# Optimization experiments

Hardware: AMD Instinct MI355X
Metric: run time of the kernel (lower is better)

## Reference

```python
import jax, jax.numpy as jnp
import numpy as np

WS = (7, 7)  # window size
NUM_HEADS = 16


def _relative_position_index(ws):
    # Deterministic int index table, computed exactly as in the torch module.
    coords = np.stack(np.meshgrid(np.arange(ws[0]), np.arange(ws[1]), indexing='ij'))  # [2,Wh,Ww]
    coords = coords.reshape(2, -1)                       # [2, N]
    rel = coords[:, :, None] - coords[:, None, :]        # [2, N, N]
    rel = rel.transpose(1, 2, 0)                         # [N, N, 2]
    rel = rel + np.array([ws[0] - 1, ws[1] - 1])
    rel[:, :, 0] *= 2 * ws[1] - 1
    return jnp.asarray(rel.sum(-1), dtype=jnp.int32)     # [N, N]


def setup_inputs() -> dict:
    key = jax.random.key(0)
    ks = jax.random.split(key, 5)
    B_, N, C = 2048, WS[0] * WS[1], 512
    nw = 64
    return {
        'x': jax.random.normal(ks[0], (B_, N, C), dtype=jnp.float32),
        'mask': jax.random.normal(ks[1], (nw, N, N), dtype=jnp.float32),
        'qkv_w': jax.random.normal(ks[2], (3 * C, C), dtype=jnp.float32) * 0.02,
        'qkv_b': jax.random.normal(ks[3], (3 * C,), dtype=jnp.float32) * 0.02,
        'rpb_table': jax.random.normal(ks[4], ((2 * WS[0] - 1) * (2 * WS[1] - 1), NUM_HEADS), dtype=jnp.float32) * 0.02,
    }


def reference(x, mask, qkv_w, qkv_b, rpb_table):
    B_, N, C = x.shape
    H = NUM_HEADS
    hd = C // H
    scale = hd ** -0.5

    # qkv projection: [B_, N, 3, H, hd] -> q, k, v each [B_, H, N, hd]
    qkv = (jnp.einsum('bnc,oc->bno', x, qkv_w) + qkv_b)
    qkv = qkv.reshape(B_, N, 3, H, hd).transpose(2, 0, 3, 1, 4)
    q, k, v = qkv[0], qkv[1], qkv[2]

    attn = jnp.einsum('bhnd,bhmd->bhnm', q * scale, k)  # [B_, H, N, N]

    rel_idx = _relative_position_index(WS)                       # [N, N]
    bias = rpb_table[rel_idx.reshape(-1)].reshape(N, N, H)       # gather
    attn = attn + bias.transpose(2, 0, 1)[None]                  # [1, H, N, N]

    nw = mask.shape[0]
    attn = attn.reshape(B_ // nw, nw, H, N, N) + mask[None, :, None]
    attn = attn.reshape(B_, H, N, N)
    attn = jax.nn.softmax(attn, axis=-1)

    out = jnp.einsum('bhnm,bhmd->bhnd', attn, v)
    out = out.transpose(0, 2, 1, 3).reshape(B_, N, C)
    # NOTE: source assigns `X = self.proj(x)` but returns `x`, so the
    # output projection is dead code; we faithfully return pre-proj output.
    return out
```

## Files before the change

### kernel.cpp

```cpp
#include <hip/hip_runtime.h>
#include <cstdint>
#include <cstddef>

typedef __bf16 bf16x8 __attribute__((ext_vector_type(8)));
typedef float f32x4 __attribute__((ext_vector_type(4)));
typedef unsigned short u16x8 __attribute__((ext_vector_type(8)));
typedef unsigned short u16x4 __attribute__((ext_vector_type(4)));
typedef unsigned int u32x2 __attribute__((ext_vector_type(2)));

#define VT_LD 56
#define LDE 144
#define BSTRIDE 52
#define BSZ 2548
#define PLD 80

__device__ __forceinline__ unsigned short f2bf(float f) {
  unsigned int u = __builtin_bit_cast(unsigned int, f);
  u += 0x7FFFu + ((u >> 16) & 1u);
  return (unsigned short)(u >> 16);
}
__device__ __forceinline__ float bf2f(unsigned short h) {
  unsigned int u = (unsigned int)h << 16;
  return __builtin_bit_cast(float, u);
}

__device__ __forceinline__ void gload_lds16(const void* g, void* l) {
  __builtin_amdgcn_global_load_lds((const __attribute__((address_space(1))) void*)g,
                                   (__attribute__((address_space(3))) void*)l, 16, 0, 0);
}

__global__ void conv_f2b_k(const float* __restrict__ src, unsigned short* __restrict__ dst, long n8) {
  long i = (long)blockIdx.x * blockDim.x + threadIdx.x;
  long stride = (long)gridDim.x * blockDim.x;
  for (; i < n8; i += stride) {
    float4 a = *(const float4*)(src + i * 8);
    float4 b = *(const float4*)(src + i * 8 + 4);
    u16x8 p;
    p[0]=f2bf(a.x); p[1]=f2bf(a.y); p[2]=f2bf(a.z); p[3]=f2bf(a.w);
    p[4]=f2bf(b.x); p[5]=f2bf(b.y); p[6]=f2bf(b.z); p[7]=f2bf(b.w);
    *(u16x8*)(dst + i * 8) = p;
  }
}

__global__ void build_bias_k(const float* __restrict__ rpb, unsigned short* __restrict__ biasT) {
  int idx = blockIdx.x * 256 + threadIdx.x;
  if (idx >= 16 * BSZ) return;
  int h = idx / BSZ;
  int rem = idx - h * BSZ;
  int i = rem / BSTRIDE, j = rem - (rem / BSTRIDE) * BSTRIDE;
  unsigned short v = 0;
  if (j < 49) {
    int r1 = i / 7, c1 = i - r1 * 7;
    int r2 = j / 7, c2 = j - r2 * 7;
    int ri = (r1 - r2 + 6) * 13 + (c1 - c2 + 6);
    v = f2bf(rpb[ri * 16 + h]);
  }
  biasT[idx] = v;
}

__global__ __launch_bounds__(256, 3) void qkv_gemm_k(
    const unsigned short* __restrict__ xb, const float* __restrict__ qkv_b,
    const unsigned short* __restrict__ wb,
    unsigned short* __restrict__ qs, unsigned short* __restrict__ kk,
    unsigned short* __restrict__ vt)
{
  __shared__ __align__(16) unsigned short smem[18432];
  unsigned short* Ab = smem;
  unsigned short* Bb = smem + 8192;

  int bid = blockIdx.x;
  int sw = (bid & 7) * 1176 + (bid >> 3);
  int mt = sw / 12, nt = sw - mt * 12;
  long m0 = (long)mt * 128;
  int  n0 = nt * 128;
  int  s  = n0 >> 9;

  int t = threadIdx.x;
  int lane = t & 63, wv = t >> 6;
  int g = lane >> 4, q = lane & 15;
  int wrow = wv >> 1, wcol = wv & 1;

  f32x4 acc[4][4] = {};

  int schunk = (t & 3) ^ ((t >> 3) & 3);
  const unsigned short* ag0 = xb + (m0 + (t >> 2)) * 512 + schunk * 8;
  const unsigned short* ag1 = ag0 + 64 * 512;
  const unsigned short* bg0 = wb + (size_t)(n0 + (t >> 2)) * 512 + schunk * 8;
  const unsigned short* bg1 = bg0 + 64 * 512;
  unsigned short* alA  = Ab + wv * 512;
  unsigned short* alA2 = Ab + 2048 + wv * 512;
  unsigned short* blB  = Bb + wv * 512;
  unsigned short* blB2 = Bb + 2048 + wv * 512;

  int roff = (8 * g) ^ (((q >> 1) & 3) << 3);
  const unsigned short* arb = Ab + (wrow * 64 + q) * 32 + roff;
  const unsigned short* brb = Bb + (wcol * 64 + q) * 32 + roff;

#define STAGE(KT, BOFF) do {                    \
    int kof = (KT) * 32;                        \
    gload_lds16(ag0 + kof, alA  + (BOFF));      \
    gload_lds16(ag1 + kof, alA2 + (BOFF));      \
    gload_lds16(bg0 + kof, blB  + (BOFF));      \
    gload_lds16(bg1 + kof, blB2 + (BOFF));      \
  } while (0)

#define COMPUTE(BOFF) do {                                                     \
    bf16x8 af[4], bfr[4];                                                      \
    _Pragma("unroll")                                                          \
    for (int i2 = 0; i2 < 4; ++i2) af[i2]  = *(const bf16x8*)(arb + (BOFF) + i2 * 512); \
    _Pragma("unroll")                                                          \
    for (int j2 = 0; j2 < 4; ++j2) bfr[j2] = *(const bf16x8*)(brb + (BOFF) + j2 * 512); \
    _Pragma("unroll")                                                          \
    for (int i2 = 0; i2 < 4; ++i2)                                             \
      _Pragma("unroll")                                                        \
      for (int j2 = 0; j2 < 4; ++j2)                                           \
        acc[i2][j2] = __builtin_amdgcn_mfma_f32_16x16x32_bf16(af[i2], bfr[j2], acc[i2][j2], 0, 0, 0); \
  } while (0)

  STAGE(0, 0);
  __syncthreads();
  for (int kt = 0; kt < 16; kt += 2) {
    STAGE(kt + 1, 4096);
    COMPUTE(0);
    __syncthreads();
    if (kt + 2 < 16) STAGE(kt + 2, 0);
    COMPUTE(4096);
    __syncthreads();
  }
#undef STAGE
#undef COMPUTE

  int   nl[4];
  float bias[4];
  #pragma unroll
  for (int j2 = 0; j2 < 4; ++j2) {
    nl[j2] = wcol * 64 + j2 * 16 + q;
    bias[j2] = qkv_b[n0 + nl[j2]];
  }

  if (s < 2) {
    float sc = (s == 0) ? 0.17677669529663687f : 1.0f;
    #pragma unroll
    for (int i2 = 0; i2 < 4; ++i2) {
      #pragma unroll
      for (int r = 0; r < 4; ++r) {
        int ml = wrow * 64 + i2 * 16 + 4 * g + r;
        #pragma unroll
        for (int j2 = 0; j2 < 4; ++j2)
          smem[ml * LDE + nl[j2]] = f2bf((acc[i2][j2][r] + bias[j2]) * sc);
      }
    }
    __syncthreads();
    unsigned short* dst = (s == 0) ? qs : kk;
    int c8 = (t & 15) * 8;
    int d0 = c8 & 31;
    int h  = ((n0 + c8) >> 5) & 15;
    #pragma unroll
    for (int p = 0; p < 8; ++p) {
      int row = p * 16 + (t >> 4);
      unsigned int gm = (unsigned int)m0 + row;
      unsigned int b  = gm / 49;
      unsigned int i  = gm - b * 49;
      u16x8 val = *(const u16x8*)(smem + row * LDE + c8);
      *(u16x8*)(dst + ((size_t)(b * 16 + h) * 49 + i) * 32 + d0) = val;
    }
  } else {
    #pragma unroll
    for (int j2 = 0; j2 < 4; ++j2) {
      int d = nl[j2] & 31;
      int h = ((n0 + nl[j2]) >> 5) & 15;
      #pragma unroll
      for (int i2 = 0; i2 < 4; ++i2) {
        unsigned int gm0 = (unsigned int)m0 + wrow * 64 + i2 * 16 + 4 * g;
        unsigned int b0 = gm0 / 49;
        unsigned int i0 = gm0 - b0 * 49;
        unsigned short hv[4];
        #pragma unroll
        for (int r = 0; r < 4; ++r) hv[r] = f2bf(acc[i2][j2][r] + bias[j2]);
        if (i0 <= 45) {
          unsigned short* base = vt + ((size_t)(b0 * 16 + h) * 32 + d) * VT_LD;
          if ((i0 & 1) == 0) {
            *(unsigned int*)(base + i0)     = (unsigned int)hv[0] | ((unsigned int)hv[1] << 16);
            *(unsigned int*)(base + i0 + 2) = (unsigned int)hv[2] | ((unsigned int)hv[3] << 16);
          } else {
            base[i0] = hv[0];
            *(unsigned int*)(base + i0 + 1) = (unsigned int)hv[1] | ((unsigned int)hv[2] << 16);
            base[i0 + 3] = hv[3];
          }
        } else {
          #pragma unroll
          for (int r = 0; r < 4; ++r) {
            unsigned int gm = gm0 + r;
            unsigned int b = gm / 49;
            unsigned int i = gm - b * 49;
            vt[((size_t)(b * 16 + h) * 32 + d) * VT_LD + i] = hv[r];
          }
        }
      }
    }
  }
}

__global__ __launch_bounds__(256, 2) void win_attn_k(
    const unsigned short* __restrict__ qs, const unsigned short* __restrict__ kk,
    const unsigned short* __restrict__ vt, const unsigned short* __restrict__ biasT,
    const float* __restrict__ mask, float* __restrict__ out)
{
  __shared__ float mlds[BSZ];
  __shared__ unsigned short plds[4][64 * PLD];

  int b = blockIdx.x;
  int t = threadIdx.x;
  int lane = t & 63, wv = t >> 6;
  int g = lane >> 4, q = lane & 15;

  const float* msrc = mask + (size_t)(b & 63) * 2401;
  for (int idx = t; idx < BSZ; idx += 256) {
    int i = idx / BSTRIDE, j = idx - (idx / BSTRIDE) * BSTRIDE;
    mlds[idx] = (j < 49) ? msrc[i * 49 + j] : 0.0f;
  }
  __syncthreads();

  unsigned short* pl = plds[wv];
  const float NINF = -__builtin_inff();

  int rc[4];
  rc[0] = q; rc[1] = 16 + q; rc[2] = 32 + q; rc[3] = 48;

  int h0 = wv * 4;
  const unsigned short* qh = qs + (size_t)(b * 16 + h0) * (49 * 32);
  const unsigned short* kh = kk + (size_t)(b * 16 + h0) * (49 * 32);
  bf16x8 ak[4], bq[4];
  #pragma unroll
  for (int jt = 0; jt < 4; ++jt) ak[jt] = *(const bf16x8*)(kh + rc[jt] * 32 + 8 * g);
  #pragma unroll
  for (int it = 0; it < 4; ++it) bq[it] = *(const bf16x8*)(qh + rc[it] * 32 + 8 * g);

  #pragma unroll
  for (int hh = 0; hh < 4; ++hh) {
    int h = wv * 4 + hh;
    const unsigned short* vh  = vt + (size_t)(b * 16 + h) * (32 * VT_LD);
    const unsigned short* bh2 = biasT + h * BSZ;

    f32x4 zero = {0.f, 0.f, 0.f, 0.f};
    f32x4 st[4][4];
    __builtin_amdgcn_s_setprio(1);
    #pragma unroll
    for (int it = 0; it < 4; ++it)
      #pragma unroll
      for (int jt = 0; jt < 4; ++jt)
        st[it][jt] = __builtin_amdgcn_mfma_f32_16x16x32_bf16(ak[jt], bq[it], zero, 0, 0, 0);
    __builtin_amdgcn_s_setprio(0);

    bf16x8 akn[4], bqn[4];
    if (hh < 3) {
      const unsigned short* qh2 = qh + 49 * 32;
      const unsigned short* kh2 = kh + 49 * 32;
      #pragma unroll
      for (int jt = 0; jt < 4; ++jt) akn[jt] = *(const bf16x8*)(kh2 + rc[jt] * 32 + 8 * g);
      #pragma unroll
      for (int it = 0; it < 4; ++it) bqn[it] = *(const bf16x8*)(qh2 + rc[it] * 32 + 8 * g);
      qh = qh2; kh = kh2;
    }
    bf16x8 bv[2][2];
    #pragma unroll
    for (int ktt = 0; ktt < 2; ++ktt)
      #pragma unroll
      for (int dt = 0; dt < 2; ++dt)
        bv[ktt][dt] = *(const bf16x8*)(vh + (dt * 16 + q) * VT_LD + ktt * 32 + 8 * g);

    #pragma unroll
    for (int it = 0; it < 4; ++it) {
      int i = it * 16 + q;
      int ic = i > 48 ? 48 : i;
      f32x4 pv4[4];
      f32x4 vm = {NINF, NINF, NINF, NINF};
      #pragma unroll
      for (int jt = 0; jt < 4; ++jt) {
        if (jt == 3 && g > 0) {
          pv4[3] = (f32x4){NINF, NINF, NINF, NINF};
        } else {
          u16x4 bu = *(const u16x4*)(bh2 + ic * BSTRIDE + jt * 16 + 4 * g);
          f32x4 m4 = *(const f32x4*)(mlds + ic * BSTRIDE + jt * 16 + 4 * g);
          f32x4 sv = st[it][jt];
          #pragma unroll
          for (int r = 0; r < 4; ++r) sv[r] += bf2f(bu[r]) + m4[r];
          if (jt == 3) {
            sv[1] = NINF; sv[2] = NINF; sv[3] = NINF;
          }
          pv4[jt] = sv;
          #pragma unroll
          for (int r = 0; r < 4; ++r) vm[r] = fmaxf(vm[r], sv[r]);
        }
      }
      float mx = fmaxf(fmaxf(vm[0], vm[1]), fmaxf(vm[2], vm[3]));
      mx = fmaxf(mx, __shfl_xor(mx, 16));
      mx = fmaxf(mx, __shfl_xor(mx, 32));
      f32x4 vs = zero;
      #pragma unroll
      for (int jt = 0; jt < 4; ++jt) {
        #pragma unroll
        for (int r = 0; r < 4; ++r) {
          float p = __expf(pv4[jt][r] - mx);
          pv4[jt][r] = p;
          vs[r] += p;
        }
      }
      float sm = (vs[0] + vs[1]) + (vs[2] + vs[3]);
      sm += __shfl_xor(sm, 16);
      sm += __shfl_xor(sm, 32);
      float rv = 1.0f / sm;
      #pragma unroll
      for (int jt = 0; jt < 4; ++jt) {
        unsigned int lo = (unsigned int)f2bf(pv4[jt][0] * rv) | ((unsigned int)f2bf(pv4[jt][1] * rv) << 16);
        unsigned int hi = (unsigned int)f2bf(pv4[jt][2] * rv) | ((unsigned int)f2bf(pv4[jt][3] * rv) << 16);
        u32x2 w = {lo, hi};
        *(u32x2*)(pl + i * PLD + jt * 16 + 4 * g) = w;
      }
    }

    f32x4 oacc[4][2] = {};
    #pragma unroll
    for (int ktt = 0; ktt < 2; ++ktt) {
      bf16x8 pa[4];
      #pragma unroll
      for (int it = 0; it < 4; ++it)
        pa[it] = *(const bf16x8*)(pl + (it * 16 + q) * PLD + ktt * 32 + 8 * g);
      __builtin_amdgcn_s_setprio(1);
      #pragma unroll
      for (int it = 0; it < 4; ++it)
        #pragma unroll
        for (int dt = 0; dt < 2; ++dt)
          oacc[it][dt] = __builtin_amdgcn_mfma_f32_16x16x32_bf16(pa[it], bv[ktt][dt], oacc[it][dt], 0, 0, 0);
      __builtin_amdgcn_s_setprio(0);
    }

    #pragma unroll
    for (int it = 0; it < 4; ++it) {
      #pragma unroll
      for (int dt = 0; dt < 2; ++dt) {
        #pragma unroll
        for (int r = 0; r < 4; ++r) {
          int i = it * 16 + 4 * g + r;
          if (i < 49) {
            int d = dt * 16 + q;
            out[(size_t)(b * 49 + i) * 512 + h * 32 + d] = oacc[it][dt][r];
          }
        }
      }
    }

    if (hh < 3) {
      #pragma unroll
      for (int jt = 0; jt < 4; ++jt) ak[jt] = akn[jt];
      #pragma unroll
      for (int it = 0; it < 4; ++it) bq[it] = bqn[it];
    }
  }
}

extern "C" void kernel_launch(void* const* d_in, const int* in_sizes, int n_in,
                              void* d_out, int out_size, void* d_ws, size_t ws_size,
                              hipStream_t stream) {
  const float* x     = (const float*)d_in[0];
  const float* mask  = (const float*)d_in[1];
  const float* qkv_w = (const float*)d_in[2];
  const float* qkv_b = (const float*)d_in[3];
  const float* rpb   = (const float*)d_in[4];
  float* out = (float*)d_out;

  const size_t QS_OFF   = 0;
  const size_t KK_OFF   = 102760448;
  const size_t VT_OFF   = 205520896;
  const size_t BIAS_OFF = 322961408;
  const size_t WB_OFF   = 323042944;
  const size_t NEED     = 324615808;
  if (ws_size < NEED) return;

  char* ws = (char*)d_ws;
  unsigned short* qsb   = (unsigned short*)(ws + QS_OFF);
  unsigned short* kkb   = (unsigned short*)(ws + KK_OFF);
  unsigned short* vtb   = (unsigned short*)(ws + VT_OFF);
  unsigned short* biasT = (unsigned short*)(ws + BIAS_OFF);
  unsigned short* wb    = (unsigned short*)(ws + WB_OFF);

  unsigned short* xb = (unsigned short*)d_out;

  conv_f2b_k<<<2048, 256, 0, stream>>>(x, xb, 6422528);
  conv_f2b_k<<<512, 256, 0, stream>>>(qkv_w, wb, 98304);
  build_bias_k<<<160, 256, 0, stream>>>(rpb, biasT);
  qkv_gemm_k<<<9408, 256, 0, stream>>>(xb, qkv_b, wb, qsb, kkb, vtb);
  win_attn_k<<<2048, 256, 0, stream>>>(qsb, kkb, vtb, biasT, mask, out);
}
```

Baseline: 441.8 us.

## Split QKV GEMM into Q/K and V kernels with swapped-operand direct epilogue

The single QKV GEMM is split into two kernels, one for the Q/K columns and one for the V columns. The Q/K kernel swaps the MFMA operands so each lane holds four consecutive output columns, and writes packed 8-byte stores straight to global memory. This removes the LDS staging round-trip and its extra barrier from the epilogue. Shared memory per block shrinks, so launch bounds rise to 4 blocks per CU for higher occupancy, at the cost of an extra kernel launch and narrower global stores.

```diff
diff --git a/kernel.cpp b/kernel.cpp
--- a/kernel.cpp
+++ b/kernel.cpp
@@ -9,7 +9,6 @@
 typedef unsigned int u32x2 __attribute__((ext_vector_type(2)));
 
 #define VT_LD 56
-#define LDE 144
 #define BSTRIDE 52
 #define BSZ 2548
 #define PLD 80
@@ -58,42 +57,23 @@
   biasT[idx] = v;
 }
 
-__global__ __launch_bounds__(256, 3) void qkv_gemm_k(
-    const unsigned short* __restrict__ xb, const float* __restrict__ qkv_b,
-    const unsigned short* __restrict__ wb,
-    unsigned short* __restrict__ qs, unsigned short* __restrict__ kk,
-    unsigned short* __restrict__ vt)
-{
-  __shared__ __align__(16) unsigned short smem[18432];
-  unsigned short* Ab = smem;
-  unsigned short* Bb = smem + 8192;
-
-  int bid = blockIdx.x;
-  int sw = (bid & 7) * 1176 + (bid >> 3);
-  int mt = sw / 12, nt = sw - mt * 12;
-  long m0 = (long)mt * 128;
-  int  n0 = nt * 128;
-  int  s  = n0 >> 9;
-
-  int t = threadIdx.x;
-  int lane = t & 63, wv = t >> 6;
-  int g = lane >> 4, q = lane & 15;
-  int wrow = wv >> 1, wcol = wv & 1;
-
-  f32x4 acc[4][4] = {};
-
-  int schunk = (t & 3) ^ ((t >> 3) & 3);
-  const unsigned short* ag0 = xb + (m0 + (t >> 2)) * 512 + schunk * 8;
-  const unsigned short* ag1 = ag0 + 64 * 512;
-  const unsigned short* bg0 = wb + (size_t)(n0 + (t >> 2)) * 512 + schunk * 8;
-  const unsigned short* bg1 = bg0 + 64 * 512;
-  unsigned short* alA  = Ab + wv * 512;
-  unsigned short* alA2 = Ab + 2048 + wv * 512;
-  unsigned short* blB  = Bb + wv * 512;
-  unsigned short* blB2 = Bb + 2048 + wv * 512;
-
-  int roff = (8 * g) ^ (((q >> 1) & 3) << 3);
-  const unsigned short* arb = Ab + (wrow * 64 + q) * 32 + roff;
+#define GEMM_SETUP(N0)                                                         \
+  int t = threadIdx.x;                                                         \
+  int lane = t & 63, wv = t >> 6;                                              \
+  int g = lane >> 4, q = lane & 15;                                            \
+  int wrow = wv >> 1, wcol = wv & 1;                                           \
+  f32x4 acc[4][4] = {};                                                        \
+  int schunk = (t & 3) ^ ((t >> 3) & 3);                                       \
+  const unsigned short* ag0 = xb + (m0 + (t >> 2)) * 512 + schunk * 8;         \
+  const unsigned short* ag1 = ag0 + 64 * 512;                                  \
+  const unsigned short* bg0 = wb + (size_t)((N0) + (t >> 2)) * 512 + schunk * 8; \
+  const unsigned short* bg1 = bg0 + 64 * 512;                                  \
+  unsigned short* alA  = Ab + wv * 512;                                        \
+  unsigned short* alA2 = Ab + 2048 + wv * 512;                                 \
+  unsigned short* blB  = Bb + wv * 512;                                        \
+  unsigned short* blB2 = Bb + 2048 + wv * 512;                                 \
+  int roff = (8 * g) ^ (((q >> 1) & 3) << 3);                                  \
+  const unsigned short* arb = Ab + (wrow * 64 + q) * 32 + roff;                \
   const unsigned short* brb = Bb + (wcol * 64 + q) * 32 + roff;
 
 #define STAGE(KT, BOFF) do {                    \
@@ -104,7 +84,7 @@
     gload_lds16(bg1 + kof, blB2 + (BOFF));      \
   } while (0)
 
-#define COMPUTE(BOFF) do {                                                     \
+#define COMPUTE(BOFF, SWAPPED) do {                                            \
     bf16x8 af[4], bfr[4];                                                      \
     _Pragma("unroll")                                                          \
     for (int i2 = 0; i2 < 4; ++i2) af[i2]  = *(const bf16x8*)(arb + (BOFF) + i2 * 512); \
@@ -114,87 +94,119 @@
     for (int i2 = 0; i2 < 4; ++i2)                                             \
       _Pragma("unroll")                                                        \
       for (int j2 = 0; j2 < 4; ++j2)                                           \
-        acc[i2][j2] = __builtin_amdgcn_mfma_f32_16x16x32_bf16(af[i2], bfr[j2], acc[i2][j2], 0, 0, 0); \
+        acc[i2][j2] = (SWAPPED)                                                \
+          ? __builtin_amdgcn_mfma_f32_16x16x32_bf16(bfr[j2], af[i2], acc[i2][j2], 0, 0, 0) \
+          : __builtin_amdgcn_mfma_f32_16x16x32_bf16(af[i2], bfr[j2], acc[i2][j2], 0, 0, 0); \
   } while (0)
 
-  STAGE(0, 0);
-  __syncthreads();
-  for (int kt = 0; kt < 16; kt += 2) {
-    STAGE(kt + 1, 4096);
-    COMPUTE(0);
-    __syncthreads();
-    if (kt + 2 < 16) STAGE(kt + 2, 0);
-    COMPUTE(4096);
-    __syncthreads();
-  }
-#undef STAGE
-#undef COMPUTE
-
-  int   nl[4];
-  float bias[4];
+#define KLOOP(SWAPPED)                          \
+  STAGE(0, 0);                                  \
+  __syncthreads();                              \
+  for (int kt = 0; kt < 16; kt += 2) {          \
+    STAGE(kt + 1, 4096);                        \
+    COMPUTE(0, SWAPPED);                        \
+    __syncthreads();                            \
+    if (kt + 2 < 16) STAGE(kt + 2, 0);          \
+    COMPUTE(4096, SWAPPED);                     \
+    __syncthreads();                            \
+  }
+
+__global__ __launch_bounds__(256, 4) void qkv_gemm_qk_k(
+    const unsigned short* __restrict__ xb, const float* __restrict__ qkv_b,
+    const unsigned short* __restrict__ wb,
+    unsigned short* __restrict__ qs, unsigned short* __restrict__ kk)
+{
+  __shared__ __align__(16) unsigned short smem[16384];
+  unsigned short* Ab = smem;
+  unsigned short* Bb = smem + 8192;
+
+  int bid = blockIdx.x;
+  int sw = (bid & 7) * 784 + (bid >> 3);
+  int mt = sw >> 3, ntl = sw & 7;
+  long m0 = (long)mt * 128;
+  int  n0 = ntl * 128;
+  int  s  = n0 >> 9;
+
+  GEMM_SETUP(n0)
+  KLOOP(1)
+
+  unsigned short* dst = (s == 0) ? qs : kk;
+  float sc = (s == 0) ? 0.17677669529663687f : 1.0f;
+  float4 bi[4];
+  int hj[4], dj[4];
   #pragma unroll
   for (int j2 = 0; j2 < 4; ++j2) {
-    nl[j2] = wcol * 64 + j2 * 16 + q;
-    bias[j2] = qkv_b[n0 + nl[j2]];
-  }
-
-  if (s < 2) {
-    float sc = (s == 0) ? 0.17677669529663687f : 1.0f;
+    int n = n0 + wcol * 64 + j2 * 16 + 4 * g;
+    bi[j2] = *(const float4*)(qkv_b + n);
+    hj[j2] = (n >> 5) & 15;
+    dj[j2] = n & 31;
+  }
+  #pragma unroll
+  for (int i2 = 0; i2 < 4; ++i2) {
+    unsigned int m = (unsigned int)m0 + wrow * 64 + i2 * 16 + q;
+    unsigned int b = m / 49;
+    unsigned int i = m - b * 49;
+    size_t base = ((size_t)(b * 16) * 49 + i) * 32;
+    #pragma unroll
+    for (int j2 = 0; j2 < 4; ++j2) {
+      f32x4 a = acc[i2][j2];
+      unsigned int lo = (unsigned int)f2bf((a[0] + bi[j2].x) * sc) | ((unsigned int)f2bf((a[1] + bi[j2].y) * sc) << 16);
+      unsigned int hi = (unsigned int)f2bf((a[2] + bi[j2].z) * sc) | ((unsigned int)f2bf((a[3] + bi[j2].w) * sc) << 16);
+      u32x2 wv2 = {lo, hi};
+      *(u32x2*)(dst + base + (size_t)hj[j2] * (49 * 32) + dj[j2]) = wv2;
+    }
+  }
+}
+
+__global__ __launch_bounds__(256, 4) void qkv_gemm_v_k(
+    const unsigned short* __restrict__ xb, const float* __restrict__ qkv_b,
+    const unsigned short* __restrict__ wb,
+    unsigned short* __restrict__ vt)
+{
+  __shared__ __align__(16) unsigned short smem[16384];
+  unsigned short* Ab = smem;
+  unsigned short* Bb = smem + 8192;
+
+  int bid = blockIdx.x;
+  int sw = (bid & 7) * 392 + (bid >> 3);
+  int mt = sw >> 2, ntv = sw & 3;
+  long m0 = (long)mt * 128;
+  int  n0 = 1024 + ntv * 128;
+
+  GEMM_SETUP(n0)
+  KLOOP(0)
+
+  #pragma unroll
+  for (int j2 = 0; j2 < 4; ++j2) {
+    int n  = n0 + wcol * 64 + j2 * 16 + q;
+    float bias = qkv_b[n];
+    int d = n & 31;
+    int h = (n >> 5) & 15;
     #pragma unroll
     for (int i2 = 0; i2 < 4; ++i2) {
-      #pragma unroll
-      for (int r = 0; r < 4; ++r) {
-        int ml = wrow * 64 + i2 * 16 + 4 * g + r;
+      unsigned int gm0 = (unsigned int)m0 + wrow * 64 + i2 * 16 + 4 * g;
+      unsigned int b0 = gm0 / 49;
+      unsigned int i0 = gm0 - b0 * 49;
+      unsigned short hv[4];
+      #pragma unroll
+      for (int r = 0; r < 4; ++r) hv[r] = f2bf(acc[i2][j2][r] + bias);
+      if (i0 <= 45) {
+        unsigned short* base = vt + ((size_t)(b0 * 16 + h) * 32 + d) * VT_LD;
+        if ((i0 & 1) == 0) {
+          *(unsigned int*)(base + i0)     = (unsigned int)hv[0] | ((unsigned int)hv[1] << 16);
+          *(unsigned int*)(base + i0 + 2) = (unsigned int)hv[2] | ((unsigned int)hv[3] << 16);
+        } else {
+          base[i0] = hv[0];
+          *(unsigned int*)(base + i0 + 1) = (unsigned int)hv[1] | ((unsigned int)hv[2] << 16);
+          base[i0 + 3] = hv[3];
+        }
+      } else {
         #pragma unroll
-        for (int j2 = 0; j2 < 4; ++j2)
-          smem[ml * LDE + nl[j2]] = f2bf((acc[i2][j2][r] + bias[j2]) * sc);
-      }
-    }
-    __syncthreads();
-    unsigned short* dst = (s == 0) ? qs : kk;
-    int c8 = (t & 15) * 8;
-    int d0 = c8 & 31;
-    int h  = ((n0 + c8) >> 5) & 15;
-    #pragma unroll
-    for (int p = 0; p < 8; ++p) {
-      int row = p * 16 + (t >> 4);
-      unsigned int gm = (unsigned int)m0 + row;
-      unsigned int b  = gm / 49;
-      unsigned int i  = gm - b * 49;
-      u16x8 val = *(const u16x8*)(smem + row * LDE + c8);
-      *(u16x8*)(dst + ((size_t)(b * 16 + h) * 49 + i) * 32 + d0) = val;
-    }
-  } else {
-    #pragma unroll
-    for (int j2 = 0; j2 < 4; ++j2) {
-      int d = nl[j2] & 31;
-      int h = ((n0 + nl[j2]) >> 5) & 15;
-      #pragma unroll
-      for (int i2 = 0; i2 < 4; ++i2) {
-        unsigned int gm0 = (unsigned int)m0 + wrow * 64 + i2 * 16 + 4 * g;
-        unsigned int b0 = gm0 / 49;
-        unsigned int i0 = gm0 - b0 * 49;
-        unsigned short hv[4];
-        #pragma unroll
-        for (int r = 0; r < 4; ++r) hv[r] = f2bf(acc[i2][j2][r] + bias[j2]);
-        if (i0 <= 45) {
-          unsigned short* base = vt + ((size_t)(b0 * 16 + h) * 32 + d) * VT_LD;
-          if ((i0 & 1) == 0) {
-            *(unsigned int*)(base + i0)     = (unsigned int)hv[0] | ((unsigned int)hv[1] << 16);
-            *(unsigned int*)(base + i0 + 2) = (unsigned int)hv[2] | ((unsigned int)hv[3] << 16);
-          } else {
-            base[i0] = hv[0];
-            *(unsigned int*)(base + i0 + 1) = (unsigned int)hv[1] | ((unsigned int)hv[2] << 16);
-            base[i0 + 3] = hv[3];
-          }
-        } else {
-          #pragma unroll
-          for (int r = 0; r < 4; ++r) {
-            unsigned int gm = gm0 + r;
-            unsigned int b = gm / 49;
-            unsigned int i = gm - b * 49;
-            vt[((size_t)(b * 16 + h) * 32 + d) * VT_LD + i] = hv[r];
-          }
+        for (int r = 0; r < 4; ++r) {
+          unsigned int gm = gm0 + r;
+          unsigned int b = gm / 49;
+          unsigned int i = gm - b * 49;
+          vt[((size_t)(b * 16 + h) * 32 + d) * VT_LD + i] = hv[r];
         }
       }
     }
@@ -389,6 +401,7 @@
   conv_f2b_k<<<2048, 256, 0, stream>>>(x, xb, 6422528);
   conv_f2b_k<<<512, 256, 0, stream>>>(qkv_w, wb, 98304);
   build_bias_k<<<160, 256, 0, stream>>>(rpb, biasT);
-  qkv_gemm_k<<<9408, 256, 0, stream>>>(xb, qkv_b, wb, qsb, kkb, vtb);
+  qkv_gemm_qk_k<<<6272, 256, 0, stream>>>(xb, qkv_b, wb, qsb, kkb);
+  qkv_gemm_v_k<<<3136, 256, 0, stream>>>(xb, qkv_b, wb, vtb);
   win_attn_k<<<2048, 256, 0, stream>>>(qsb, kkb, vtb, biasT, mask, out);
 }
```

After: 475.6 us. +7.6%, slower.
